# Kernel tuning notes

Hardware: AMD Instinct MI355X
Metric: run time of the kernel (lower is better)

The kernel has to match this reference:

```python
import jax, jax.numpy as jnp
import numpy as np

TAU = 2.0      # spikingjelly LIFNode default tau
V_TH = 1.0     # default v_threshold
ALPHA = 4.0    # default surrogate.Sigmoid alpha


@jax.custom_vjp
def spike_fn(v):
    # Heaviside(v - v_th) with sigmoid surrogate gradient
    return (v >= V_TH).astype(v.dtype)

def _spike_fwd(v):
    return (v >= V_TH).astype(v.dtype), v

def _spike_bwd(v, g):
    s = jax.nn.sigmoid(ALPHA * (v - V_TH))
    return (g * ALPHA * s * (1.0 - s),)

spike_fn.defvjp(_spike_fwd, _spike_bwd)


def lif(x):
    """Multi-step LIF: decay_input=False, hard reset to v_reset=0, detach_reset.
    x: [T, B, C, N] -> spikes [T, B, C, N]."""
    def step(v, xt):
        v = v * (1.0 - 1.0 / TAU) + xt          # v = v - (v - 0)/tau + x
        s = spike_fn(v)
        v = v * (1.0 - jax.lax.stop_gradient(s))  # hard reset, detached spike
        return v, s
    v0 = jnp.zeros_like(x[0])
    _, spikes = jax.lax.scan(step, v0, x)
    return spikes


def setup_inputs() -> dict:
    key = jax.random.key(0)
    kx, k1, k2, k3 = jax.random.split(key, 4)
    T, B, C, dim = 4, 32, 196, 768
    scale = dim ** -0.5
    x = jax.random.normal(kx, (T, B, C, dim), dtype=jnp.float32)
    w1 = jax.random.normal(k1, (dim, dim), dtype=jnp.float32) * scale
    w2 = jax.random.normal(k2, (dim, dim), dtype=jnp.float32) * scale
    w3 = jax.random.normal(k3, (dim, dim), dtype=jnp.float32) * scale
    return {"x": x, "w1": w1, "w2": w2, "w3": w3}


def reference(x, w1, w2, w3):
    # y1 = mlp1(mlp1_lif(x)); y2 = mlp2(mlp2_lif(x)); out = mlp3(y1 * mlp3_lif(y2))
    y1 = jnp.einsum('tbcn,mn->tbcm', lif(x), w1)
    y2 = jnp.einsum('tbcn,mn->tbcm', lif(x), w2)
    out = jnp.einsum('tbcn,mn->tbcm', y1 * lif(y2), w3)
    return out
```

## Files before the change

kernel.cpp:

```cpp
#include <hip/hip_runtime.h>
#include <stdint.h>

#define T_STEPS 4
#define BC      6272
#define NDIM    768
#define TBC     (T_STEPS*BC)
#define BCN     (BC*NDIM)
#define FIX_CAP 65536

typedef unsigned short u16;
typedef __attribute__((ext_vector_type(8))) __bf16 bf16x8;
typedef __attribute__((ext_vector_type(4))) float f32x4;
typedef __attribute__((ext_vector_type(4))) int   i32x4;

#define MFMA16(a,b,c)  __builtin_amdgcn_mfma_f32_16x16x32_bf16((a),(b),(c),0,0,0)
#define MFMAI8(a,b,c)  __builtin_amdgcn_mfma_i32_16x16x64_i8((a),(b),(c),0,0,0)

__device__ __forceinline__ u16 f2b(float f) {
    uint32_t u = __builtin_bit_cast(uint32_t, f);
    u += 0x7FFFu + ((u >> 16) & 1u);
    return (u16)(u >> 16);
}
__device__ __forceinline__ void gload16(const void* g, void* l) {
    __builtin_amdgcn_global_load_lds((const __attribute__((address_space(1))) void*)g,
                                     (__attribute__((address_space(3))) void*)l,
                                     16, 0, 0);
}

__global__ __launch_bounds__(256) void front_kernel(
    const float* __restrict__ x,
    const float* __restrict__ w1, const float* __restrict__ w2,
    const float* __restrict__ w3,
    int8_t* __restrict__ s8, u16* __restrict__ cnt,
    int8_t* __restrict__ w1q, int8_t* __restrict__ w2h,
    int8_t* __restrict__ w2l, u16* __restrict__ w3b,
    uint32_t* __restrict__ fix_cnt)
{
    if (blockIdx.x < BC / 4) {
        const int bc   = blockIdx.x * 4 + (threadIdx.x >> 6);
        const int lane = threadIdx.x & 63;
        const size_t base = (size_t)bc * NDIM + lane * 12;

        double v[12];
        #pragma unroll
        for (int j = 0; j < 12; ++j) v[j] = 0.0;
        uint32_t c01 = 0, c23 = 0;

        #pragma unroll
        for (int t = 0; t < T_STEPS; ++t) {
            float4 xa = *(const float4*)&x[(size_t)t * BCN + base + 0];
            float4 xb = *(const float4*)&x[(size_t)t * BCN + base + 4];
            float4 xc = *(const float4*)&x[(size_t)t * BCN + base + 8];
            float xs[12] = {xa.x, xa.y, xa.z, xa.w, xb.x, xb.y, xb.z, xb.w,
                            xc.x, xc.y, xc.z, xc.w};
            uint32_t pk[3] = {0, 0, 0};
            uint32_t csum = 0;
            #pragma unroll
            for (int j = 0; j < 12; ++j) {
                v[j] = 0.5 * v[j] + (double)xs[j];
                if (v[j] >= 1.0) {
                    pk[j >> 2] |= 1u << ((j & 3) * 8);
                    csum++;
                    v[j] = 0.0;
                }
            }
            uint32_t* dst = (uint32_t*)&s8[(size_t)t * BCN + base];
            dst[0] = pk[0]; dst[1] = pk[1]; dst[2] = pk[2];
            if (t < 2) c01 += csum << (t * 16);
            else       c23 += csum << ((t - 2) * 16);
        }
        #pragma unroll
        for (int o = 32; o > 0; o >>= 1) {
            c01 += __shfl_xor(c01, o);
            c23 += __shfl_xor(c23, o);
        }
        if (lane == 0) {
            cnt[0 * BC + bc] = (u16)(c01 & 0xFFFF);
            cnt[1 * BC + bc] = (u16)(c01 >> 16);
            cnt[2 * BC + bc] = (u16)(c23 & 0xFFFF);
            cnt[3 * BC + bc] = (u16)(c23 >> 16);
        }
    } else {
        int i = (blockIdx.x - BC / 4) * 256 + threadIdx.x;
        if (i == 0) *fix_cnt = 0;
        int q1 = __float2int_rn(w1[i] * 512.0f);
        q1 = q1 > 127 ? 127 : (q1 < -127 ? -127 : q1);
        w1q[i] = (int8_t)q1;
        int q16 = __double2int_rn((double)w2[i] * 65536.0);
        int8_t lo = (int8_t)(q16 & 0xFF);
        int hi = (q16 - (int)lo) >> 8;
        w2h[i] = (int8_t)hi;
        w2l[i] = lo;
        w3b[i] = f2b(w3[i]);
    }
}

__global__ __launch_bounds__(256) void y12_kernel(
    const int8_t* __restrict__ s8,
    const int8_t* __restrict__ w1q, const int8_t* __restrict__ w2hb,
    const int8_t* __restrict__ w2lb,
    const u16* __restrict__ cnt,
    u16* __restrict__ z,
    uint32_t* __restrict__ fix_cnt,
    int2* __restrict__ fix_idx, float4* __restrict__ fix_y1)
{
    __shared__ int8_t lds[2][40960];

    const int tid  = threadIdx.x;
    const int lane = tid & 63;
    const int wid  = tid >> 6;

    const int bid = blockIdx.x;
    const int swz = (bid & 7) * 294 + (bid >> 3);
    const int mb  = swz % (NDIM / 64);
    const int rb  = swz / (NDIM / 64);
    const int m0  = mb * 64;
    const int bc0 = rb * 32;

    const int srow  = lane >> 3;
    const int scolB = ((lane & 7) << 4) ^ (srow << 4);
    const int8_t* gp[10];
    int lofs[10];
    #pragma unroll
    for (int c = 0; c < 10; ++c) {
        int chunk = wid * 10 + c;
        const int8_t* g;
        int l;
        if (chunk < 16) {
            int gr = chunk * 8 + srow;
            int t = gr >> 5, bcl = gr & 31;
            g = s8 + ((size_t)(t * BC + bc0 + bcl)) * NDIM + scolB;
            l = chunk * 1024;
        } else if (chunk < 24) {
            int mr = (chunk - 16) * 8 + srow;
            g = w1q + ((size_t)(m0 + mr)) * NDIM + scolB;
            l = 16384 + (chunk - 16) * 1024;
        } else if (chunk < 32) {
            int mr = (chunk - 24) * 8 + srow;
            g = w2hb + ((size_t)(m0 + mr)) * NDIM + scolB;
            l = 24576 + (chunk - 24) * 1024;
        } else {
            int mr = (chunk - 32) * 8 + srow;
            g = w2lb + ((size_t)(m0 + mr)) * NDIM + scolB;
            l = 32768 + (chunk - 32) * 1024;
        }
        gp[c] = g;
        lofs[c] = l;
    }

    const int key = lane & 7;
    const int g4  = lane >> 4;
    int slotA[2];
    slotA[0] = ((g4       ^ key) << 4);
    slotA[1] = (((4 | g4) ^ key) << 4);
    int abase[8];
    #pragma unroll
    for (int t = 0; t < 4; ++t)
        #pragma unroll
        for (int rt = 0; rt < 2; ++rt)
            abase[t * 2 + rt] = (t * 32 + rt * 16 + (lane & 15)) * 128;
    const int bbase = (wid * 16 + (lane & 15)) * 128;

    i32x4 acc1[4][2], acch[4][2], accl[4][2];
    #pragma unroll
    for (int t = 0; t < 4; ++t)
        #pragma unroll
        for (int rt = 0; rt < 2; ++rt) {
            acc1[t][rt] = (i32x4){0, 0, 0, 0};
            acch[t][rt] = (i32x4){0, 0, 0, 0};
            accl[t][rt] = (i32x4){0, 0, 0, 0};
        }

    auto stage = [&](int buf) {
        #pragma unroll
        for (int c = 0; c < 10; ++c) {
            gload16(gp[c], &lds[buf][lofs[c]]);
            gp[c] += 128;
        }
    };
    auto compute = [&](int buf) {
        const int8_t* L = lds[buf];
        #pragma unroll
        for (int ks = 0; ks < 2; ++ks) {
            const int sl = slotA[ks];
            i32x4 b1 = *(const i32x4*)&L[16384 + bbase + sl];
            i32x4 bh = *(const i32x4*)&L[24576 + bbase + sl];
            i32x4 bl = *(const i32x4*)&L[32768 + bbase + sl];
            #pragma unroll
            for (int t = 0; t < 4; ++t)
                #pragma unroll
                for (int rt = 0; rt < 2; ++rt) {
                    i32x4 a = *(const i32x4*)&L[abase[t * 2 + rt] + sl];
                    acc1[t][rt] = MFMAI8(a, b1, acc1[t][rt]);
                    acch[t][rt] = MFMAI8(a, bh, acch[t][rt]);
                    accl[t][rt] = MFMAI8(a, bl, accl[t][rt]);
                }
        }
    };

    stage(0);
    __syncthreads();
    #pragma unroll
    for (int it = 0; it < 5; ++it) {
        stage((it + 1) & 1);
        compute(it & 1);
        __syncthreads();
    }
    compute(1);

    const int mg = m0 + wid * 16 + (lane & 15);
    #pragma unroll
    for (int rt = 0; rt < 2; ++rt) {
        #pragma unroll
        for (int r = 0; r < 4; ++r) {
            const int bcg = bc0 + rt * 16 + (lane >> 4) * 4 + r;
            double v = 0.0, e = 0.0;
            bool flag = false;
            float zv[4], y1v[4];
            #pragma unroll
            for (int t = 0; t < 4; ++t) {
                float y1 = (float)acc1[t][rt][r] * (1.0f / 512.0f);
                y1v[t] = y1;
                double y2 = (double)(acch[t][rt][r] * 256 + accl[t][rt][r])
                            * (1.0 / 65536.0);
                v = 0.5 * v + y2;
                e = 0.5 * e + 7.62939453125e-6 * (double)cnt[t * BC + bcg] + 1e-9;
                double d = v - 1.0;
                flag |= (d <= e && d >= -e);
                if (v >= 1.0) { zv[t] = y1; v = 0.0; e = 0.0; }
                else          { zv[t] = 0.0f; }
            }
            if (flag) {
                uint32_t id = atomicAdd(fix_cnt, 1u);
                if (id < FIX_CAP) {
                    fix_idx[id] = make_int2(bcg, mg);
                    fix_y1[id]  = make_float4(y1v[0], y1v[1], y1v[2], y1v[3]);
                }
            }
            #pragma unroll
            for (int t = 0; t < 4; ++t)
                z[((size_t)(t * BC + bcg)) * NDIM + mg] = f2b(zv[t]);
        }
    }
}

__global__ __launch_bounds__(256) void fixup_kernel(
    const int8_t* __restrict__ s8, const float* __restrict__ w2,
    const int2* __restrict__ fix_idx, const float4* __restrict__ fix_y1,
    const uint32_t* __restrict__ fix_cnt, u16* __restrict__ z)
{
    const int lane = threadIdx.x & 63;
    const int wave = (blockIdx.x * 256 + threadIdx.x) >> 6;
    const int nw   = gridDim.x * 4;
    uint32_t n = *fix_cnt;
    if (n > FIX_CAP) n = FIX_CAP;

    for (uint32_t e = wave; e < n; e += nw) {
        const int bc = fix_idx[e].x, m = fix_idx[e].y;
        const float* w2row = w2 + (size_t)m * NDIM;
        double acc[4] = {0.0, 0.0, 0.0, 0.0};
        #pragma unroll
        for (int j = 0; j < NDIM / 64; ++j) {
            int nn = lane + j * 64;
            double wv = (double)w2row[nn];
            #pragma unroll
            for (int t = 0; t < 4; ++t)
                if (s8[((size_t)(t * BC + bc)) * NDIM + nn]) acc[t] += wv;
        }
        #pragma unroll
        for (int o = 32; o > 0; o >>= 1)
            #pragma unroll
            for (int t = 0; t < 4; ++t) acc[t] += __shfl_xor(acc[t], o);
        if (lane == 0) {
            float4 y1 = fix_y1[e];
            float y1a[4] = {y1.x, y1.y, y1.z, y1.w};
            double v = 0.0;
            #pragma unroll
            for (int t = 0; t < 4; ++t) {
                v = 0.5 * v + acc[t];
                u16 zz = 0;
                if (v >= 1.0) { zz = f2b(y1a[t]); v = 0.0; }
                z[((size_t)(t * BC + bc)) * NDIM + m] = zz;
            }
        }
    }
}

__global__ __launch_bounds__(256, 2) void out_kernel(
    const u16* __restrict__ z, const u16* __restrict__ w3b,
    float* __restrict__ out)
{
    __shared__ u16 lds[2][16384];

    const int lane = threadIdx.x & 63;
    const int wid  = threadIdx.x >> 6;
    const int rw   = wid >> 1;
    const int cw   = wid & 1;

    const int bid = blockIdx.x;
    const int swz = (bid & 7) * 147 + (bid >> 3);
    const int mb  = swz % (NDIM / 128);
    const int rb  = swz / (NDIM / 128);
    const int m0  = mb * 128;
    const int r0  = rb * 128;

    const int srow  = lane >> 3;
    const int scolE = ((((lane & 7) << 4) ^ ((srow & 7) << 4)) >> 1);
    const u16* gp[8];
    int lofs[8];
    #pragma unroll
    for (int c = 0; c < 8; ++c) {
        int chunk = wid * 8 + c;
        const u16* g;
        if (chunk < 16) {
            int gr = chunk * 8 + srow;
            g = z + ((size_t)(r0 + gr)) * NDIM + scolE;
        } else {
            int mr = (chunk - 16) * 8 + srow;
            g = w3b + ((size_t)(m0 + mr)) * NDIM + scolE;
        }
        gp[c] = g;
        lofs[c] = chunk * 512;
    }

    const int swzb = (lane & 7) << 4;
    const int cb   = (lane >> 4) << 4;
    const int colE0 = ((cb     ) ^ swzb) >> 1;
    const int colE1 = ((cb | 64) ^ swzb) >> 1;

    f32x4 acc[4][4];
    #pragma unroll
    for (int rt = 0; rt < 4; ++rt)
        #pragma unroll
        for (int cf = 0; cf < 4; ++cf) acc[rt][cf] = (f32x4){0.f, 0.f, 0.f, 0.f};

    auto stage = [&](int buf) {
        #pragma unroll
        for (int c = 0; c < 8; ++c) {
            gload16(gp[c], &lds[buf][lofs[c]]);
            gp[c] += 64;
        }
    };
    auto compute = [&](int buf) {
        const u16* L = lds[buf];
        #pragma unroll
        for (int k2i = 0; k2i < 2; ++k2i) {
            const int ce = k2i ? colE1 : colE0;
            bf16x8 bw[4];
            #pragma unroll
            for (int cf = 0; cf < 4; ++cf)
                bw[cf] = *(const bf16x8*)&L[8192 + (cw * 64 + cf * 16 + (lane & 15)) * 64 + ce];
            #pragma unroll
            for (int rt = 0; rt < 4; ++rt) {
                bf16x8 az = *(const bf16x8*)&L[(rw * 64 + rt * 16 + (lane & 15)) * 64 + ce];
                #pragma unroll
                for (int cf = 0; cf < 4; ++cf)
                    acc[rt][cf] = MFMA16(az, bw[cf], acc[rt][cf]);
            }
        }
    };

    stage(0);
    __syncthreads();
    for (int it = 0; it < 11; ++it) {
        stage((it + 1) & 1);
        compute(it & 1);
        __syncthreads();
    }
    compute(1);

    #pragma unroll
    for (int rt = 0; rt < 4; ++rt)
        #pragma unroll
        for (int cf = 0; cf < 4; ++cf)
            #pragma unroll
            for (int r = 0; r < 4; ++r)
                out[((size_t)(r0 + rw * 64 + rt * 16 + (lane >> 4) * 4 + r)) * NDIM
                    + m0 + cw * 64 + cf * 16 + (lane & 15)] = acc[rt][cf][r];
}

extern "C" void kernel_launch(void* const* d_in, const int* in_sizes, int n_in,
                              void* d_out, int out_size, void* d_ws, size_t ws_size,
                              hipStream_t stream) {
    const float* x  = (const float*)d_in[0];
    const float* w1 = (const float*)d_in[1];
    const float* w2 = (const float*)d_in[2];
    const float* w3 = (const float*)d_in[3];
    float* out = (float*)d_out;

    char* ws = (char*)d_ws;
    int8_t*   s8      = (int8_t*)(ws);
    u16*      z       = (u16*)(ws + 19267584);
    int8_t*   w1q     = (int8_t*)(ws + 57802752);
    int8_t*   w2h     = (int8_t*)(ws + 58392576);
    int8_t*   w2l     = (int8_t*)(ws + 58982400);
    u16*      w3b     = (u16*)(ws + 59572224);
    u16*      cnt     = (u16*)(ws + 60751872);
    uint32_t* fix_cnt = (uint32_t*)(ws + 60802048);
    int2*     fix_idx = (int2*)(ws + 60802112);
    float4*   fix_y1  = (float4*)(ws + 61326400);

    front_kernel<<<BC / 4 + (NDIM * NDIM) / 256, 256, 0, stream>>>(
        x, w1, w2, w3, s8, cnt, w1q, w2h, w2l, w3b, fix_cnt);
    y12_kernel<<<(BC / 32) * (NDIM / 64), 256, 0, stream>>>(s8, w1q, w2h, w2l,
                                                            cnt, z, fix_cnt,
                                                            fix_idx, fix_y1);
    fixup_kernel<<<512, 256, 0, stream>>>(s8, w2, fix_idx, fix_y1, fix_cnt, z);
    out_kernel<<<(TBC / 128) * (NDIM / 128), 256, 0, stream>>>(z, w3b, out);
}
```

Baseline: 121.9 us.

## Split y12 GEMM into two kernels, second half using 32x32 int8 MFMA tiles

The y12 stage is split into two launches. The original 64-column-tile kernel handles the first half of the row blocks. A new variant handles the second half with 128-column tiles and 32x32x32 int8 MFMA instructions, reusing each LDS fragment across more output and issuing fewer instructions. The two launches run back to back on the same stream, which adds launch overhead and a possible tail gap between them. It is most likely an A/B experiment on the tile shape.

Result: slower. 152.5 us (+25.0%).

```diff
diff --git a/kernel.cpp b/kernel.cpp
--- a/kernel.cpp
+++ b/kernel.cpp
@@ -10,11 +10,13 @@
 
 typedef unsigned short u16;
 typedef __attribute__((ext_vector_type(8))) __bf16 bf16x8;
-typedef __attribute__((ext_vector_type(4))) float f32x4;
-typedef __attribute__((ext_vector_type(4))) int   i32x4;
-
-#define MFMA16(a,b,c)  __builtin_amdgcn_mfma_f32_16x16x32_bf16((a),(b),(c),0,0,0)
-#define MFMAI8(a,b,c)  __builtin_amdgcn_mfma_i32_16x16x64_i8((a),(b),(c),0,0,0)
+typedef __attribute__((ext_vector_type(4)))  float f32x4;
+typedef __attribute__((ext_vector_type(4)))  int   i32x4;
+typedef __attribute__((ext_vector_type(16))) int   i32x16;
+
+#define MFMA16(a,b,c)    __builtin_amdgcn_mfma_f32_16x16x32_bf16((a),(b),(c),0,0,0)
+#define MFMAI8(a,b,c)    __builtin_amdgcn_mfma_i32_16x16x64_i8((a),(b),(c),0,0,0)
+#define MFMAI8_32(a,b,c) __builtin_amdgcn_mfma_i32_32x32x32_i8((a),(b),(c),0,0,0)
 
 __device__ __forceinline__ u16 f2b(float f) {
     uint32_t u = __builtin_bit_cast(uint32_t, f);
@@ -95,25 +97,25 @@
     }
 }
 
-__global__ __launch_bounds__(256) void y12_kernel(
+__global__ __launch_bounds__(256) void y12_v1(
     const int8_t* __restrict__ s8,
     const int8_t* __restrict__ w1q, const int8_t* __restrict__ w2hb,
     const int8_t* __restrict__ w2lb,
     const u16* __restrict__ cnt,
     u16* __restrict__ z,
     uint32_t* __restrict__ fix_cnt,
-    int2* __restrict__ fix_idx, float4* __restrict__ fix_y1)
+    int2* __restrict__ fix_idx, float4* __restrict__ fix_y1,
+    int rb_base)
 {
     __shared__ int8_t lds[2][40960];
 
-    const int tid  = threadIdx.x;
-    const int lane = tid & 63;
-    const int wid  = tid >> 6;
+    const int lane = threadIdx.x & 63;
+    const int wid  = threadIdx.x >> 6;
 
     const int bid = blockIdx.x;
-    const int swz = (bid & 7) * 294 + (bid >> 3);
+    const int swz = (bid & 7) * 147 + (bid >> 3);
     const int mb  = swz % (NDIM / 64);
-    const int rb  = swz / (NDIM / 64);
+    const int rb  = rb_base + swz / (NDIM / 64);
     const int m0  = mb * 64;
     const int bc0 = rb * 32;
 
@@ -244,6 +246,140 @@
     }
 }
 
+__global__ __launch_bounds__(256) void y12_v2(
+    const int8_t* __restrict__ s8,
+    const int8_t* __restrict__ w1q, const int8_t* __restrict__ w2hb,
+    const int8_t* __restrict__ w2lb,
+    const u16* __restrict__ cnt,
+    u16* __restrict__ z,
+    uint32_t* __restrict__ fix_cnt,
+    int2* __restrict__ fix_idx, float4* __restrict__ fix_y1,
+    int rb_base)
+{
+    __shared__ int8_t lds[2][32768];
+
+    const int lane = threadIdx.x & 63;
+    const int wid  = threadIdx.x >> 6;
+
+    const int bid = blockIdx.x;
+    const int mb  = bid % (NDIM / 128);
+    const int rb  = rb_base + bid / (NDIM / 128);
+    const int m0  = mb * 128;
+    const int bc0 = rb * 32;
+
+    const int scolB = ((lane & 3) ^ ((lane >> 3) & 3)) << 4;
+    const int srow  = lane >> 2;
+    const int8_t* gp[8];
+    int lofs[8];
+    #pragma unroll
+    for (int c = 0; c < 8; ++c) {
+        int chunk = wid * 8 + c;
+        const int8_t* g;
+        int l;
+        if (chunk < 8) {
+            int gr = chunk * 16 + srow;
+            int t = gr >> 5, bcl = gr & 31;
+            g = s8 + ((size_t)(t * BC + bc0 + bcl)) * NDIM + scolB;
+            l = chunk * 1024;
+        } else if (chunk < 16) {
+            int mr = (chunk - 8) * 16 + srow;
+            g = w1q + ((size_t)(m0 + mr)) * NDIM + scolB;
+            l = 8192 + (chunk - 8) * 1024;
+        } else if (chunk < 24) {
+            int mr = (chunk - 16) * 16 + srow;
+            g = w2hb + ((size_t)(m0 + mr)) * NDIM + scolB;
+            l = 16384 + (chunk - 16) * 1024;
+        } else {
+            int mr = (chunk - 24) * 16 + srow;
+            g = w2lb + ((size_t)(m0 + mr)) * NDIM + scolB;
+            l = 24576 + (chunk - 24) * 1024;
+        }
+        gp[c] = g;
+        lofs[c] = l;
+    }
+
+    const int rloc = lane & 31;
+    const int half = lane >> 5;
+    const int k2   = (lane >> 1) & 3;
+    const int sl0  = ((half      ^ k2) << 4);
+    const int sl1  = (((2 | half) ^ k2) << 4);
+    const int arow = rloc * 64;
+    const int brow = (wid * 32 + rloc) * 64;
+
+    i32x16 a1[4], ah[4], al[4];
+    #pragma unroll
+    for (int t = 0; t < 4; ++t) {
+        a1[t] = (i32x16)(0);
+        ah[t] = (i32x16)(0);
+        al[t] = (i32x16)(0);
+    }
+
+    auto stage = [&](int buf) {
+        #pragma unroll
+        for (int c = 0; c < 8; ++c) {
+            gload16(gp[c], &lds[buf][lofs[c]]);
+            gp[c] += 64;
+        }
+    };
+    auto compute = [&](int buf) {
+        const int8_t* L = lds[buf];
+        #pragma unroll
+        for (int ks = 0; ks < 2; ++ks) {
+            const int sl = ks ? sl1 : sl0;
+            i32x4 b1 = *(const i32x4*)&L[ 8192 + brow + sl];
+            i32x4 bh = *(const i32x4*)&L[16384 + brow + sl];
+            i32x4 bl = *(const i32x4*)&L[24576 + brow + sl];
+            #pragma unroll
+            for (int t = 0; t < 4; ++t) {
+                i32x4 a = *(const i32x4*)&L[arow + t * 2048 + sl];
+                a1[t] = MFMAI8_32(a, b1, a1[t]);
+                ah[t] = MFMAI8_32(a, bh, ah[t]);
+                al[t] = MFMAI8_32(a, bl, al[t]);
+            }
+        }
+    };
+
+    stage(0);
+    __syncthreads();
+    for (int it = 0; it < 11; ++it) {
+        stage((it + 1) & 1);
+        compute(it & 1);
+        __syncthreads();
+    }
+    compute(1);
+
+    const int mg = m0 + wid * 32 + rloc;
+    #pragma unroll
+    for (int r = 0; r < 16; ++r) {
+        const int bcg = bc0 + (r & 3) + ((r >> 2) << 3) + (half << 2);
+        double v = 0.0, e = 0.0;
+        bool flag = false;
+        float zv[4], y1v[4];
+        #pragma unroll
+        for (int t = 0; t < 4; ++t) {
+            float y1 = (float)a1[t][r] * (1.0f / 512.0f);
+            y1v[t] = y1;
+            double y2 = (double)(ah[t][r] * 256 + al[t][r]) * (1.0 / 65536.0);
+            v = 0.5 * v + y2;
+            e = 0.5 * e + 7.62939453125e-6 * (double)cnt[t * BC + bcg] + 1e-9;
+            double d = v - 1.0;
+            flag |= (d <= e && d >= -e);
+            if (v >= 1.0) { zv[t] = y1; v = 0.0; e = 0.0; }
+            else          { zv[t] = 0.0f; }
+        }
+        if (flag) {
+            uint32_t id = atomicAdd(fix_cnt, 1u);
+            if (id < FIX_CAP) {
+                fix_idx[id] = make_int2(bcg, mg);
+                fix_y1[id]  = make_float4(y1v[0], y1v[1], y1v[2], y1v[3]);
+            }
+        }
+        #pragma unroll
+        for (int t = 0; t < 4; ++t)
+            z[((size_t)(t * BC + bcg)) * NDIM + mg] = f2b(zv[t]);
+    }
+}
+
 __global__ __launch_bounds__(256) void fixup_kernel(
     const int8_t* __restrict__ s8, const float* __restrict__ w2,
     const int2* __restrict__ fix_idx, const float4* __restrict__ fix_y1,
@@ -402,9 +538,10 @@
 
     front_kernel<<<BC / 4 + (NDIM * NDIM) / 256, 256, 0, stream>>>(
         x, w1, w2, w3, s8, cnt, w1q, w2h, w2l, w3b, fix_cnt);
-    y12_kernel<<<(BC / 32) * (NDIM / 64), 256, 0, stream>>>(s8, w1q, w2h, w2l,
-                                                            cnt, z, fix_cnt,
-                                                            fix_idx, fix_y1);
+    y12_v1<<<1176, 256, 0, stream>>>(s8, w1q, w2h, w2l, cnt, z, fix_cnt,
+                                     fix_idx, fix_y1, 0);
+    y12_v2<<<588, 256, 0, stream>>>(s8, w1q, w2h, w2l, cnt, z, fix_cnt,
+                                    fix_idx, fix_y1, 98);
     fixup_kernel<<<512, 256, 0, stream>>>(s8, w2, fix_idx, fix_y1, fix_cnt, z);
     out_kernel<<<(TBC / 128) * (NDIM / 128), 256, 0, stream>>>(z, w3b, out);
 }
```
